# Optimization experiments

Hardware: AMD Instinct MI355X
Metric: run time of the kernel (lower is better)

## Reference

```python
import jax, jax.numpy as jnp
import numpy as np

B, P, Q, E, V = 8192, 24, 12, 256, 1000
LN_EPS = 1e-5


def setup_inputs() -> dict:
    key = jax.random.key(0)
    ks = jax.random.split(key, 9)
    s1 = 1.0  # Linear(1,E): fan_in=1 -> kaiming uniform bound = 1
    s2 = 1.0 / np.sqrt(E)
    return {
        "x_num": jax.random.normal(ks[0], (B, P), dtype=jnp.float32),
        "x_cat": jax.random.randint(ks[1], (B, Q), 0, V, dtype=jnp.int64),
        "W1": jax.random.uniform(ks[2], (P, E), jnp.float32, -s1, s1),   # per-attr Linear(1,E) weight
        "b1": jax.random.uniform(ks[3], (P, E), jnp.float32, -s1, s1),
        "W2": jax.random.uniform(ks[4], (P, E, E), jnp.float32, -s2, s2),  # per-attr Linear(E,E)
        "b2": jax.random.uniform(ks[5], (P, E), jnp.float32, -s2, s2),
        "emb": jax.random.normal(ks[6], (Q, V, E), dtype=jnp.float32),   # per-attr embedding tables
        "gamma": jnp.ones((E,), jnp.float32),
        "beta": jnp.zeros((E,), jnp.float32),
    }


def reference(x_num, x_cat, W1, b1, W2, b2, emb, gamma, beta):
    # Numeric attrs: scalar -> E (Linear), GELU, E -> E (Linear), all P attrs batched.
    h = x_num[:, :, None] * W1[None, :, :] + b1[None, :, :]           # [B,P,E]
    h = jax.nn.gelu(h, approximate=False)                              # torch nn.GELU default (erf)
    num_tok = jnp.einsum("bpe,pef->bpf", h, W2) + b2[None, :, :]     # [B,P,E]
    # Categorical attrs: per-attribute gather.
    cat_tok = emb[jnp.arange(Q)[None, :], x_cat]                       # [B,Q,E]
    tokens = jnp.concatenate([num_tok, cat_tok], axis=1)               # [B,P+Q,E]
    # LayerNorm over last dim.
    mu = jnp.mean(tokens, axis=-1, keepdims=True)
    var = jnp.mean(jnp.square(tokens - mu), axis=-1, keepdims=True)
    return (tokens - mu) * jax.lax.rsqrt(var + LN_EPS) * gamma + beta
```

## Files before the change

kernel.cpp:

```cpp
#include <hip/hip_runtime.h>
#include <hip/hip_bf16.h>
#include <math.h>

#define B_ 8192
#define P_ 24
#define Q_ 12
#define E_ 256
#define V_ 1000
#define TOK_ 36
#define NK_ 129
#define NI_ 128
#define KT_ 8
#define NKBLK_ 17
#define X0_ (-6.0f)
#define DX_ (12.0f / 128.0f)
#define INVDX_ (128.0f / 12.0f)
#define LN_EPS_ 1e-5f

typedef float vfloat4 __attribute__((ext_vector_type(4)));

__device__ __forceinline__ float gelu_exact(float u) {
    return 0.5f * u * (1.0f + erff(u * 0.70710678118654752f));
}

__global__ __launch_bounds__(256) void build_table(
        const float* __restrict__ W1, const float* __restrict__ b1,
        const float* __restrict__ W2, const float* __restrict__ b2,
        float* __restrict__ T) {
    int p = blockIdx.x / NKBLK_;
    int k0 = (blockIdx.x - p * NKBLK_) * KT_;
    int f = threadIdx.x;

    __shared__ float h[KT_][E_ + 4];

    float w = W1[p * E_ + f];
    float b1v = b1[p * E_ + f];
    #pragma unroll
    for (int k = 0; k < KT_; ++k) {
        float x = X0_ + (float)(k0 + k) * DX_;
        h[k][f] = gelu_exact(fmaf(x, w, b1v));
    }
    __syncthreads();

    float acc[KT_];
    float b2v = b2[p * E_ + f];
    #pragma unroll
    for (int k = 0; k < KT_; ++k) acc[k] = b2v;

    const float* W2p = W2 + (size_t)p * E_ * E_ + f;
    for (int e = 0; e < E_; e += 4) {
        float w0 = W2p[(size_t)(e + 0) * E_];
        float w1 = W2p[(size_t)(e + 1) * E_];
        float w2v = W2p[(size_t)(e + 2) * E_];
        float w3 = W2p[(size_t)(e + 3) * E_];
        #pragma unroll
        for (int k = 0; k < KT_; ++k) {
            float4 hv = *(const float4*)&h[k][e];
            acc[k] = fmaf(hv.x, w0, acc[k]);
            acc[k] = fmaf(hv.y, w1, acc[k]);
            acc[k] = fmaf(hv.z, w2v, acc[k]);
            acc[k] = fmaf(hv.w, w3, acc[k]);
        }
    }
    #pragma unroll
    for (int k = 0; k < KT_; ++k) {
        int kk = k0 + k;
        if (kk < NK_) T[((size_t)p * NK_ + kk) * E_ + f] = acc[k];
    }
}

__device__ __forceinline__ void ln_store(float4 v, float4 g, float4 bt, int e0, int row,
                                         float* __restrict__ out) {
    float s1 = v.x + v.y + v.z + v.w;
    #pragma unroll
    for (int m = 1; m < 64; m <<= 1) s1 += __shfl_xor(s1, m, 64);
    float mean = s1 * (1.0f / (float)E_);
    float dx = v.x - mean, dy = v.y - mean, dz = v.z - mean, dw = v.w - mean;
    float s2 = dx * dx + dy * dy + dz * dz + dw * dw;
    #pragma unroll
    for (int m = 1; m < 64; m <<= 1) s2 += __shfl_xor(s2, m, 64);
    float rstd = rsqrtf(s2 * (1.0f / (float)E_) + LN_EPS_);
    vfloat4 o;
    o.x = fmaf(dx * rstd, g.x, bt.x);
    o.y = fmaf(dy * rstd, g.y, bt.y);
    o.z = fmaf(dz * rstd, g.z, bt.z);
    o.w = fmaf(dw * rstd, g.w, bt.w);
    __builtin_nontemporal_store(o, (vfloat4*)&out[(size_t)row * E_ + e0]);
}

__global__ __launch_bounds__(256) void fuse_all(
        const float* __restrict__ T,
        const float* __restrict__ x_num, const int* __restrict__ x_cat,
        const float* __restrict__ emb,
        const float* __restrict__ gamma, const float* __restrict__ beta,
        float* __restrict__ out) {
    int wv = threadIdx.x >> 6;
    int lane = threadIdx.x & 63;
    int base = (blockIdx.x * 4 + wv) * 4;
    int b = base / TOK_;
    int t0 = base - b * TOK_;
    int e0 = lane * 4;

    float4 g = *(const float4*)&gamma[e0];
    float4 bt = *(const float4*)&beta[e0];

    float4 v[4];
    if (t0 < P_) {
        float4 x4 = *(const float4*)&x_num[b * P_ + t0];
        float xs[4] = {x4.x, x4.y, x4.z, x4.w};
        const float* bases[4];
        float tts[4];
        #pragma unroll
        for (int j = 0; j < 4; ++j) {
            float s = (xs[j] - X0_) * INVDX_;
            float fi = floorf(s);
            fi = fminf(fmaxf(fi, 0.0f), (float)(NI_ - 1));
            tts[j] = s - fi;
            bases[j] = T + ((size_t)(t0 + j) * NK_ + (int)fi) * E_ + e0;
        }
        float4 a[4], c[4];
        #pragma unroll
        for (int j = 0; j < 4; ++j) {
            a[j] = *(const float4*)bases[j];
            c[j] = *(const float4*)(bases[j] + E_);
        }
        #pragma unroll
        for (int j = 0; j < 4; ++j) {
            v[j].x = fmaf(tts[j], c[j].x - a[j].x, a[j].x);
            v[j].y = fmaf(tts[j], c[j].y - a[j].y, a[j].y);
            v[j].z = fmaf(tts[j], c[j].z - a[j].z, a[j].z);
            v[j].w = fmaf(tts[j], c[j].w - a[j].w, a[j].w);
        }
    } else {
        int q0 = t0 - P_;
        int4 id4 = *(const int4*)&x_cat[b * Q_ + q0];
        int ids[4] = {id4.x, id4.y, id4.z, id4.w};
        #pragma unroll
        for (int j = 0; j < 4; ++j)
            v[j] = *(const float4*)&emb[((size_t)(q0 + j) * V_ + ids[j]) * E_ + e0];
    }
    #pragma unroll
    for (int j = 0; j < 4; ++j) ln_store(v[j], g, bt, e0, base + j, out);
}

__global__ __launch_bounds__(256) void fuse_exact(
        const float* __restrict__ x_num, const int* __restrict__ x_cat,
        const float* __restrict__ W1, const float* __restrict__ b1,
        const float* __restrict__ W2, const float* __restrict__ b2,
        const float* __restrict__ emb,
        const float* __restrict__ gamma, const float* __restrict__ beta,
        float* __restrict__ out) {
    int wv = threadIdx.x >> 6;
    int lane = threadIdx.x & 63;
    int row = blockIdx.x * 4 + wv;
    if (row >= B_ * TOK_) return;
    int b = row / TOK_;
    int t = row - b * TOK_;
    int e0 = lane * 4;
    float4 g = *(const float4*)&gamma[e0];
    float4 bt = *(const float4*)&beta[e0];
    float4 v;
    if (t < P_) {
        float x = x_num[b * P_ + t];
        float4 acc = *(const float4*)&b2[t * E_ + e0];
        for (int e = 0; e < E_; ++e) {
            float he = gelu_exact(fmaf(x, W1[t * E_ + e], b1[t * E_ + e]));
            float4 w = *(const float4*)&W2[((size_t)t * E_ + e) * E_ + e0];
            acc.x = fmaf(he, w.x, acc.x);
            acc.y = fmaf(he, w.y, acc.y);
            acc.z = fmaf(he, w.z, acc.z);
            acc.w = fmaf(he, w.w, acc.w);
        }
        v = acc;
    } else {
        int q = t - P_;
        int idx = x_cat[b * Q_ + q];
        v = *(const float4*)&emb[((size_t)q * V_ + idx) * E_ + e0];
    }
    ln_store(v, g, bt, e0, row, out);
}

extern "C" void kernel_launch(void* const* d_in, const int* in_sizes, int n_in,
                              void* d_out, int out_size, void* d_ws, size_t ws_size,
                              hipStream_t stream) {
    const float* x_num = (const float*)d_in[0];
    const int*   x_cat = (const int*)d_in[1];
    const float* W1    = (const float*)d_in[2];
    const float* b1    = (const float*)d_in[3];
    const float* W2    = (const float*)d_in[4];
    const float* b2    = (const float*)d_in[5];
    const float* emb   = (const float*)d_in[6];
    const float* gamma = (const float*)d_in[7];
    const float* beta  = (const float*)d_in[8];
    float* out = (float*)d_out;

    size_t tbl_bytes = (size_t)P_ * NK_ * E_ * sizeof(float);

    if (ws_size >= tbl_bytes) {
        float* Tbl = (float*)d_ws;
        build_table<<<P_ * NKBLK_, 256, 0, stream>>>(W1, b1, W2, b2, Tbl);
        int nblocks = (B_ * TOK_) / 16;
        fuse_all<<<nblocks, 256, 0, stream>>>(Tbl, x_num, x_cat, emb, gamma, beta, out);
    } else {
        int nrow_blocks = (B_ * TOK_ + 3) / 4;
        fuse_exact<<<nrow_blocks, 256, 0, stream>>>(x_num, x_cat, W1, b1, W2, b2,
                                                    emb, gamma, beta, out);
    }
}
```

Measured before the change: 83.74 us.

## Precompute LayerNorm statistics per table interval and embedding row

Per-row LayerNorm statistics are now precomputed. Each embedding row gets its sum and sum of squares, and each interpolation interval gets the moments sa, sc, saa, scc and sac, so the main kernel computes mean and variance in closed form without wave-wide shuffle reductions. The main kernel becomes a grid-stride loop over 2048 blocks, and the embedding stats are computed inside the table-build launch. This adds one extra kernel launch and an E[x^2]-mean^2 variance formula that is less numerically robust, in exchange for removing the per-row shuffle reductions.

New measurement: 86.89 us. 3.8% more time.

```diff
diff --git a/kernel.cpp b/kernel.cpp
--- a/kernel.cpp
+++ b/kernel.cpp
@@ -12,10 +12,15 @@
 #define NI_ 128
 #define KT_ 8
 #define NKBLK_ 17
+#define NBUILD_ (P_ * NKBLK_)
+#define NEMBROW_ (Q_ * V_)
+#define NEMB_BLK_ ((NEMBROW_ + 3) / 4)
+#define NTILE_ ((B_ * TOK_) / 16)
 #define X0_ (-6.0f)
 #define DX_ (12.0f / 128.0f)
 #define INVDX_ (128.0f / 12.0f)
 #define LN_EPS_ 1e-5f
+#define INV_E_ (1.0f / 256.0f)
 
 typedef float vfloat4 __attribute__((ext_vector_type(4)));
 
@@ -23,124 +28,166 @@
     return 0.5f * u * (1.0f + erff(u * 0.70710678118654752f));
 }
 
-__global__ __launch_bounds__(256) void build_table(
+__device__ __forceinline__ float wave_sum(float x) {
+    #pragma unroll
+    for (int m = 1; m < 64; m <<= 1) x += __shfl_xor(x, m, 64);
+    return x;
+}
+
+__global__ __launch_bounds__(256) void build_and_embstats(
         const float* __restrict__ W1, const float* __restrict__ b1,
         const float* __restrict__ W2, const float* __restrict__ b2,
-        float* __restrict__ T) {
-    int p = blockIdx.x / NKBLK_;
-    int k0 = (blockIdx.x - p * NKBLK_) * KT_;
-    int f = threadIdx.x;
-
+        const float* __restrict__ emb,
+        float* __restrict__ T, float* __restrict__ ES) {
     __shared__ float h[KT_][E_ + 4];
 
-    float w = W1[p * E_ + f];
-    float b1v = b1[p * E_ + f];
-    #pragma unroll
-    for (int k = 0; k < KT_; ++k) {
-        float x = X0_ + (float)(k0 + k) * DX_;
-        h[k][f] = gelu_exact(fmaf(x, w, b1v));
-    }
-    __syncthreads();
-
-    float acc[KT_];
-    float b2v = b2[p * E_ + f];
-    #pragma unroll
-    for (int k = 0; k < KT_; ++k) acc[k] = b2v;
-
-    const float* W2p = W2 + (size_t)p * E_ * E_ + f;
-    for (int e = 0; e < E_; e += 4) {
-        float w0 = W2p[(size_t)(e + 0) * E_];
-        float w1 = W2p[(size_t)(e + 1) * E_];
-        float w2v = W2p[(size_t)(e + 2) * E_];
-        float w3 = W2p[(size_t)(e + 3) * E_];
+    if (blockIdx.x < NBUILD_) {
+        int p = blockIdx.x / NKBLK_;
+        int k0 = (blockIdx.x - p * NKBLK_) * KT_;
+        int f = threadIdx.x;
+
+        float w = W1[p * E_ + f];
+        float b1v = b1[p * E_ + f];
         #pragma unroll
         for (int k = 0; k < KT_; ++k) {
-            float4 hv = *(const float4*)&h[k][e];
-            acc[k] = fmaf(hv.x, w0, acc[k]);
-            acc[k] = fmaf(hv.y, w1, acc[k]);
-            acc[k] = fmaf(hv.z, w2v, acc[k]);
-            acc[k] = fmaf(hv.w, w3, acc[k]);
-        }
-    }
-    #pragma unroll
-    for (int k = 0; k < KT_; ++k) {
-        int kk = k0 + k;
-        if (kk < NK_) T[((size_t)p * NK_ + kk) * E_ + f] = acc[k];
-    }
-}
-
-__device__ __forceinline__ void ln_store(float4 v, float4 g, float4 bt, int e0, int row,
-                                         float* __restrict__ out) {
-    float s1 = v.x + v.y + v.z + v.w;
-    #pragma unroll
-    for (int m = 1; m < 64; m <<= 1) s1 += __shfl_xor(s1, m, 64);
-    float mean = s1 * (1.0f / (float)E_);
-    float dx = v.x - mean, dy = v.y - mean, dz = v.z - mean, dw = v.w - mean;
-    float s2 = dx * dx + dy * dy + dz * dz + dw * dw;
-    #pragma unroll
-    for (int m = 1; m < 64; m <<= 1) s2 += __shfl_xor(s2, m, 64);
-    float rstd = rsqrtf(s2 * (1.0f / (float)E_) + LN_EPS_);
-    vfloat4 o;
-    o.x = fmaf(dx * rstd, g.x, bt.x);
-    o.y = fmaf(dy * rstd, g.y, bt.y);
-    o.z = fmaf(dz * rstd, g.z, bt.z);
-    o.w = fmaf(dw * rstd, g.w, bt.w);
-    __builtin_nontemporal_store(o, (vfloat4*)&out[(size_t)row * E_ + e0]);
-}
-
-__global__ __launch_bounds__(256) void fuse_all(
-        const float* __restrict__ T,
+            float x = X0_ + (float)(k0 + k) * DX_;
+            h[k][f] = gelu_exact(fmaf(x, w, b1v));
+        }
+        __syncthreads();
+
+        float acc[KT_];
+        float b2v = b2[p * E_ + f];
+        #pragma unroll
+        for (int k = 0; k < KT_; ++k) acc[k] = b2v;
+
+        const float* W2p = W2 + (size_t)p * E_ * E_ + f;
+        for (int e = 0; e < E_; e += 4) {
+            float w0 = W2p[(size_t)(e + 0) * E_];
+            float w1 = W2p[(size_t)(e + 1) * E_];
+            float w2v = W2p[(size_t)(e + 2) * E_];
+            float w3 = W2p[(size_t)(e + 3) * E_];
+            #pragma unroll
+            for (int k = 0; k < KT_; ++k) {
+                float4 hv = *(const float4*)&h[k][e];
+                acc[k] = fmaf(hv.x, w0, acc[k]);
+                acc[k] = fmaf(hv.y, w1, acc[k]);
+                acc[k] = fmaf(hv.z, w2v, acc[k]);
+                acc[k] = fmaf(hv.w, w3, acc[k]);
+            }
+        }
+        #pragma unroll
+        for (int k = 0; k < KT_; ++k) {
+            int kk = k0 + k;
+            if (kk < NK_) T[((size_t)p * NK_ + kk) * E_ + f] = acc[k];
+        }
+    } else {
+        int wv = threadIdx.x >> 6;
+        int lane = threadIdx.x & 63;
+        int r = (blockIdx.x - NBUILD_) * 4 + wv;
+        if (r >= NEMBROW_) return;
+        float4 e4 = *(const float4*)&emb[(size_t)r * E_ + lane * 4];
+        float s1 = e4.x + e4.y + e4.z + e4.w;
+        float s2 = e4.x * e4.x + e4.y * e4.y + e4.z * e4.z + e4.w * e4.w;
+        s1 = wave_sum(s1);
+        s2 = wave_sum(s2);
+        if (lane == 0) { ES[r * 2] = s1; ES[r * 2 + 1] = s2; }
+    }
+}
+
+__global__ __launch_bounds__(256) void interval_stats(
+        const float* __restrict__ T, float* __restrict__ IS) {
+    int wv = threadIdx.x >> 6;
+    int lane = threadIdx.x & 63;
+    int m = blockIdx.x * 4 + wv;
+    if (m >= P_ * NI_) return;
+    int p = m >> 7;
+    int i = m & 127;
+    const float* rowa = T + ((size_t)p * NK_ + i) * E_ + lane * 4;
+    float4 a = *(const float4*)rowa;
+    float4 c = *(const float4*)(rowa + E_);
+    float sa = a.x + a.y + a.z + a.w;
+    float sc = c.x + c.y + c.z + c.w;
+    float saa = a.x * a.x + a.y * a.y + a.z * a.z + a.w * a.w;
+    float scc = c.x * c.x + c.y * c.y + c.z * c.z + c.w * c.w;
+    float sac = a.x * c.x + a.y * c.y + a.z * c.z + a.w * c.w;
+    sa = wave_sum(sa); sc = wave_sum(sc);
+    saa = wave_sum(saa); scc = wave_sum(scc); sac = wave_sum(sac);
+    if (lane == 0) {
+        float* o = IS + (size_t)m * 8;
+        o[0] = sa; o[1] = sc; o[2] = saa; o[3] = scc; o[4] = sac;
+        o[5] = 0.f; o[6] = 0.f; o[7] = 0.f;
+    }
+}
+
+__global__ __launch_bounds__(256) void fuse_stream(
+        const float* __restrict__ T, const float* __restrict__ IS,
+        const float* __restrict__ ES,
         const float* __restrict__ x_num, const int* __restrict__ x_cat,
         const float* __restrict__ emb,
         const float* __restrict__ gamma, const float* __restrict__ beta,
         float* __restrict__ out) {
     int wv = threadIdx.x >> 6;
     int lane = threadIdx.x & 63;
-    int base = (blockIdx.x * 4 + wv) * 4;
-    int b = base / TOK_;
-    int t0 = base - b * TOK_;
     int e0 = lane * 4;
-
     float4 g = *(const float4*)&gamma[e0];
     float4 bt = *(const float4*)&beta[e0];
 
-    float4 v[4];
-    if (t0 < P_) {
-        float4 x4 = *(const float4*)&x_num[b * P_ + t0];
-        float xs[4] = {x4.x, x4.y, x4.z, x4.w};
-        const float* bases[4];
-        float tts[4];
-        #pragma unroll
-        for (int j = 0; j < 4; ++j) {
-            float s = (xs[j] - X0_) * INVDX_;
-            float fi = floorf(s);
-            fi = fminf(fmaxf(fi, 0.0f), (float)(NI_ - 1));
-            tts[j] = s - fi;
-            bases[j] = T + ((size_t)(t0 + j) * NK_ + (int)fi) * E_ + e0;
-        }
-        float4 a[4], c[4];
-        #pragma unroll
-        for (int j = 0; j < 4; ++j) {
-            a[j] = *(const float4*)bases[j];
-            c[j] = *(const float4*)(bases[j] + E_);
-        }
-        #pragma unroll
-        for (int j = 0; j < 4; ++j) {
-            v[j].x = fmaf(tts[j], c[j].x - a[j].x, a[j].x);
-            v[j].y = fmaf(tts[j], c[j].y - a[j].y, a[j].y);
-            v[j].z = fmaf(tts[j], c[j].z - a[j].z, a[j].z);
-            v[j].w = fmaf(tts[j], c[j].w - a[j].w, a[j].w);
-        }
-    } else {
-        int q0 = t0 - P_;
-        int4 id4 = *(const int4*)&x_cat[b * Q_ + q0];
-        int ids[4] = {id4.x, id4.y, id4.z, id4.w};
-        #pragma unroll
-        for (int j = 0; j < 4; ++j)
-            v[j] = *(const float4*)&emb[((size_t)(q0 + j) * V_ + ids[j]) * E_ + e0];
-    }
-    #pragma unroll
-    for (int j = 0; j < 4; ++j) ln_store(v[j], g, bt, e0, base + j, out);
+    for (int tile = blockIdx.x; tile < NTILE_; tile += gridDim.x) {
+        int base = tile * 16 + wv * 4;
+        int b = base / TOK_;
+        int t0 = base - b * TOK_;
+        if (t0 < P_) {
+            float4 x4 = *(const float4*)&x_num[b * P_ + t0];
+            float xs[4] = {x4.x, x4.y, x4.z, x4.w};
+            #pragma unroll
+            for (int j = 0; j < 4; ++j) {
+                float s = (xs[j] - X0_) * INVDX_;
+                float fi = floorf(s);
+                fi = fminf(fmaxf(fi, 0.0f), (float)(NI_ - 1));
+                float t = s - fi;
+                int i = (int)fi;
+                int pp = t0 + j;
+                const float* rowa = T + ((size_t)pp * NK_ + i) * E_ + e0;
+                float4 a = *(const float4*)rowa;
+                float4 c = *(const float4*)(rowa + E_);
+                const float* ist = IS + ((size_t)pp * NI_ + i) * 8;
+                float4 q1 = *(const float4*)ist;
+                float sac = ist[4];
+                float u = 1.0f - t;
+                float mean = fmaf(t, q1.y - q1.x, q1.x) * INV_E_;
+                float m2 = (u * u * q1.z + 2.0f * t * u * sac + t * t * q1.w) * INV_E_;
+                float rstd = rsqrtf(fmaxf(m2 - mean * mean, 0.0f) + LN_EPS_);
+                vfloat4 o;
+                float vx = fmaf(t, c.x - a.x, a.x);
+                float vy = fmaf(t, c.y - a.y, a.y);
+                float vz = fmaf(t, c.z - a.z, a.z);
+                float vw = fmaf(t, c.w - a.w, a.w);
+                o.x = fmaf((vx - mean) * rstd, g.x, bt.x);
+                o.y = fmaf((vy - mean) * rstd, g.y, bt.y);
+                o.z = fmaf((vz - mean) * rstd, g.z, bt.z);
+                o.w = fmaf((vw - mean) * rstd, g.w, bt.w);
+                __builtin_nontemporal_store(o, (vfloat4*)&out[(size_t)(base + j) * E_ + e0]);
+            }
+        } else {
+            int q0 = t0 - P_;
+            int4 id4 = *(const int4*)&x_cat[b * Q_ + q0];
+            int ids[4] = {id4.x, id4.y, id4.z, id4.w};
+            #pragma unroll
+            for (int j = 0; j < 4; ++j) {
+                int r = (q0 + j) * V_ + ids[j];
+                float4 e4 = *(const float4*)&emb[(size_t)r * E_ + e0];
+                float s1 = ES[r * 2], s2 = ES[r * 2 + 1];
+                float mean = s1 * INV_E_;
+                float rstd = rsqrtf(fmaxf(s2 * INV_E_ - mean * mean, 0.0f) + LN_EPS_);
+                vfloat4 o;
+                o.x = fmaf((e4.x - mean) * rstd, g.x, bt.x);
+                o.y = fmaf((e4.y - mean) * rstd, g.y, bt.y);
+                o.z = fmaf((e4.z - mean) * rstd, g.z, bt.z);
+                o.w = fmaf((e4.w - mean) * rstd, g.w, bt.w);
+                __builtin_nontemporal_store(o, (vfloat4*)&out[(size_t)(base + j) * E_ + e0]);
+            }
+        }
+    }
 }
 
 __global__ __launch_bounds__(256) void fuse_exact(
@@ -177,7 +224,17 @@
         int idx = x_cat[b * Q_ + q];
         v = *(const float4*)&emb[((size_t)q * V_ + idx) * E_ + e0];
     }
-    ln_store(v, g, bt, e0, row, out);
+    float s1 = wave_sum(v.x + v.y + v.z + v.w);
+    float mean = s1 * INV_E_;
+    float dx = v.x - mean, dy = v.y - mean, dz = v.z - mean, dw = v.w - mean;
+    float s2 = wave_sum(dx * dx + dy * dy + dz * dz + dw * dw);
+    float rstd = rsqrtf(s2 * INV_E_ + LN_EPS_);
+    vfloat4 o;
+    o.x = fmaf(dx * rstd, g.x, bt.x);
+    o.y = fmaf(dy * rstd, g.y, bt.y);
+    o.z = fmaf(dz * rstd, g.z, bt.z);
+    o.w = fmaf(dw * rstd, g.w, bt.w);
+    __builtin_nontemporal_store(o, (vfloat4*)&out[(size_t)row * E_ + e0]);
 }
 
 extern "C" void kernel_launch(void* const* d_in, const int* in_sizes, int n_in,
@@ -194,13 +251,20 @@
     const float* beta  = (const float*)d_in[8];
     float* out = (float*)d_out;
 
-    size_t tbl_bytes = (size_t)P_ * NK_ * E_ * sizeof(float);
-
-    if (ws_size >= tbl_bytes) {
+    size_t tbl_floats = (size_t)P_ * NK_ * E_;
+    size_t is_floats  = (size_t)P_ * NI_ * 8;
+    size_t es_floats  = (size_t)NEMBROW_ * 2;
+    size_t need = (tbl_floats + is_floats + es_floats) * sizeof(float);
+
+    if (ws_size >= need) {
         float* Tbl = (float*)d_ws;
-        build_table<<<P_ * NKBLK_, 256, 0, stream>>>(W1, b1, W2, b2, Tbl);
-        int nblocks = (B_ * TOK_) / 16;
-        fuse_all<<<nblocks, 256, 0, stream>>>(Tbl, x_num, x_cat, emb, gamma, beta, out);
+        float* IS  = Tbl + tbl_floats;
+        float* ES  = IS + is_floats;
+        build_and_embstats<<<NBUILD_ + NEMB_BLK_, 256, 0, stream>>>(
+            W1, b1, W2, b2, emb, Tbl, ES);
+        interval_stats<<<(P_ * NI_) / 4, 256, 0, stream>>>(Tbl, IS);
+        fuse_stream<<<2048, 256, 0, stream>>>(Tbl, IS, ES, x_num, x_cat, emb,
+                                              gamma, beta, out);
     } else {
         int nrow_blocks = (B_ * TOK_ + 3) / 4;
         fuse_exact<<<nrow_blocks, 256, 0, stream>>>(x_num, x_cat, W1, b1, W2, b2,
```

## Overlap table build with categorical rows via cooperative persistent kernel

Applied to the files above, without the earlier changes.

Merges the table-build and fuse kernels into one cooperative persistent kernel. Some blocks build the interpolation table while the rest handle the categorical embedding rows, then a grid-wide sync precedes the numeric interpolation rows. This hides the table build behind the gather-bound categorical work and removes one launch. In exchange it adds a grid barrier, host-side attribute queries on every call, and a grid of 1024 blocks that must all be co-resident.

Result: slower. 224.2 us (+167.7%).

```diff
diff --git a/kernel.cpp b/kernel.cpp
--- a/kernel.cpp
+++ b/kernel.cpp
@@ -1,4 +1,5 @@
 #include <hip/hip_runtime.h>
+#include <hip/hip_cooperative_groups.h>
 #include <hip/hip_bf16.h>
 #include <math.h>
 
@@ -12,10 +13,15 @@
 #define NI_ 128
 #define KT_ 8
 #define NKBLK_ 17
+#define NBUILD_ (P_ * NKBLK_)
+#define NCAT_TILES_ ((B_ * Q_) / 16)
+#define NNUM_TILES_ ((B_ * P_) / 16)
+#define GRID_ 1024
 #define X0_ (-6.0f)
 #define DX_ (12.0f / 128.0f)
 #define INVDX_ (128.0f / 12.0f)
 #define LN_EPS_ 1e-5f
+#define INV_E_ (1.0f / 256.0f)
 
 typedef float vfloat4 __attribute__((ext_vector_type(4)));
 
@@ -23,15 +29,33 @@
     return 0.5f * u * (1.0f + erff(u * 0.70710678118654752f));
 }
 
-__global__ __launch_bounds__(256) void build_table(
-        const float* __restrict__ W1, const float* __restrict__ b1,
-        const float* __restrict__ W2, const float* __restrict__ b2,
-        float* __restrict__ T) {
-    int p = blockIdx.x / NKBLK_;
-    int k0 = (blockIdx.x - p * NKBLK_) * KT_;
+__device__ __forceinline__ float wave_sum(float x) {
+    #pragma unroll
+    for (int m = 1; m < 64; m <<= 1) x += __shfl_xor(x, m, 64);
+    return x;
+}
+
+__device__ __forceinline__ void ln_store(float4 v, float4 g, float4 bt, int e0, int row,
+                                         float* __restrict__ out) {
+    float mean = wave_sum(v.x + v.y + v.z + v.w) * INV_E_;
+    float dx = v.x - mean, dy = v.y - mean, dz = v.z - mean, dw = v.w - mean;
+    float s2 = wave_sum(dx * dx + dy * dy + dz * dz + dw * dw);
+    float rstd = rsqrtf(s2 * INV_E_ + LN_EPS_);
+    vfloat4 o;
+    o.x = fmaf(dx * rstd, g.x, bt.x);
+    o.y = fmaf(dy * rstd, g.y, bt.y);
+    o.z = fmaf(dz * rstd, g.z, bt.z);
+    o.w = fmaf(dw * rstd, g.w, bt.w);
+    __builtin_nontemporal_store(o, (vfloat4*)&out[(size_t)row * E_ + e0]);
+}
+
+__device__ __forceinline__ void do_build_chunk(
+        int bid, const float* __restrict__ W1, const float* __restrict__ b1,
+        const float* __restrict__ W2, const float* __restrict__ b2,
+        float* __restrict__ T, float (*h)[E_ + 4]) {
+    int p = bid / NKBLK_;
+    int k0 = (bid - p * NKBLK_) * KT_;
     int f = threadIdx.x;
-
-    __shared__ float h[KT_][E_ + 4];
 
     float w = W1[p * E_ + f];
     float b1v = b1[p * E_ + f];
@@ -69,78 +93,117 @@
     }
 }
 
-__device__ __forceinline__ void ln_store(float4 v, float4 g, float4 bt, int e0, int row,
-                                         float* __restrict__ out) {
-    float s1 = v.x + v.y + v.z + v.w;
-    #pragma unroll
-    for (int m = 1; m < 64; m <<= 1) s1 += __shfl_xor(s1, m, 64);
-    float mean = s1 * (1.0f / (float)E_);
-    float dx = v.x - mean, dy = v.y - mean, dz = v.z - mean, dw = v.w - mean;
-    float s2 = dx * dx + dy * dy + dz * dz + dw * dw;
-    #pragma unroll
-    for (int m = 1; m < 64; m <<= 1) s2 += __shfl_xor(s2, m, 64);
-    float rstd = rsqrtf(s2 * (1.0f / (float)E_) + LN_EPS_);
-    vfloat4 o;
-    o.x = fmaf(dx * rstd, g.x, bt.x);
-    o.y = fmaf(dy * rstd, g.y, bt.y);
-    o.z = fmaf(dz * rstd, g.z, bt.z);
-    o.w = fmaf(dw * rstd, g.w, bt.w);
-    __builtin_nontemporal_store(o, (vfloat4*)&out[(size_t)row * E_ + e0]);
-}
-
-__global__ __launch_bounds__(256) void fuse_all(
-        const float* __restrict__ T,
+__device__ __forceinline__ void do_cat_tile(
+        int tile, int wv, int lane, const int* __restrict__ x_cat,
+        const float* __restrict__ emb, float4 g, float4 bt,
+        float* __restrict__ out) {
+    int r0 = tile * 16 + wv * 4;
+    int b = r0 / Q_;
+    int q0 = r0 - b * Q_;
+    int e0 = lane * 4;
+    int4 id4 = *(const int4*)&x_cat[b * Q_ + q0];
+    int ids[4] = {id4.x, id4.y, id4.z, id4.w};
+    float4 v[4];
+    #pragma unroll
+    for (int j = 0; j < 4; ++j)
+        v[j] = *(const float4*)&emb[((size_t)(q0 + j) * V_ + ids[j]) * E_ + e0];
+    int orow = b * TOK_ + P_ + q0;
+    #pragma unroll
+    for (int j = 0; j < 4; ++j) ln_store(v[j], g, bt, e0, orow + j, out);
+}
+
+__device__ __forceinline__ void do_num_tile(
+        int tile, int wv, int lane, const float* __restrict__ T,
+        const float* __restrict__ x_num, float4 g, float4 bt,
+        float* __restrict__ out) {
+    int r0 = tile * 16 + wv * 4;
+    int b = r0 / P_;
+    int t0 = r0 - b * P_;
+    int e0 = lane * 4;
+    float4 x4 = *(const float4*)&x_num[b * P_ + t0];
+    float xs[4] = {x4.x, x4.y, x4.z, x4.w};
+    const float* bases[4];
+    float tts[4];
+    #pragma unroll
+    for (int j = 0; j < 4; ++j) {
+        float s = (xs[j] - X0_) * INVDX_;
+        float fi = floorf(s);
+        fi = fminf(fmaxf(fi, 0.0f), (float)(NI_ - 1));
+        tts[j] = s - fi;
+        bases[j] = T + ((size_t)(t0 + j) * NK_ + (int)fi) * E_ + e0;
+    }
+    float4 a[4], c[4];
+    #pragma unroll
+    for (int j = 0; j < 4; ++j) {
+        a[j] = *(const float4*)bases[j];
+        c[j] = *(const float4*)(bases[j] + E_);
+    }
+    int orow = b * TOK_ + t0;
+    #pragma unroll
+    for (int j = 0; j < 4; ++j) {
+        float4 v;
+        v.x = fmaf(tts[j], c[j].x - a[j].x, a[j].x);
+        v.y = fmaf(tts[j], c[j].y - a[j].y, a[j].y);
+        v.z = fmaf(tts[j], c[j].z - a[j].z, a[j].z);
+        v.w = fmaf(tts[j], c[j].w - a[j].w, a[j].w);
+        ln_store(v, g, bt, e0, orow + j, out);
+    }
+}
+
+__global__ __launch_bounds__(256, 4) void mega(
+        const float* __restrict__ W1, const float* __restrict__ b1,
+        const float* __restrict__ W2, const float* __restrict__ b2,
         const float* __restrict__ x_num, const int* __restrict__ x_cat,
         const float* __restrict__ emb,
         const float* __restrict__ gamma, const float* __restrict__ beta,
-        float* __restrict__ out) {
-    int wv = threadIdx.x >> 6;
-    int lane = threadIdx.x & 63;
-    int base = (blockIdx.x * 4 + wv) * 4;
-    int b = base / TOK_;
-    int t0 = base - b * TOK_;
-    int e0 = lane * 4;
-
+        float* __restrict__ T, float* __restrict__ out) {
+    __shared__ float h[KT_][E_ + 4];
+    int wv = threadIdx.x >> 6;
+    int lane = threadIdx.x & 63;
+    int e0 = lane * 4;
     float4 g = *(const float4*)&gamma[e0];
     float4 bt = *(const float4*)&beta[e0];
 
-    float4 v[4];
-    if (t0 < P_) {
-        float4 x4 = *(const float4*)&x_num[b * P_ + t0];
-        float xs[4] = {x4.x, x4.y, x4.z, x4.w};
-        const float* bases[4];
-        float tts[4];
-        #pragma unroll
-        for (int j = 0; j < 4; ++j) {
-            float s = (xs[j] - X0_) * INVDX_;
-            float fi = floorf(s);
-            fi = fminf(fmaxf(fi, 0.0f), (float)(NI_ - 1));
-            tts[j] = s - fi;
-            bases[j] = T + ((size_t)(t0 + j) * NK_ + (int)fi) * E_ + e0;
-        }
-        float4 a[4], c[4];
-        #pragma unroll
-        for (int j = 0; j < 4; ++j) {
-            a[j] = *(const float4*)bases[j];
-            c[j] = *(const float4*)(bases[j] + E_);
-        }
-        #pragma unroll
-        for (int j = 0; j < 4; ++j) {
-            v[j].x = fmaf(tts[j], c[j].x - a[j].x, a[j].x);
-            v[j].y = fmaf(tts[j], c[j].y - a[j].y, a[j].y);
-            v[j].z = fmaf(tts[j], c[j].z - a[j].z, a[j].z);
-            v[j].w = fmaf(tts[j], c[j].w - a[j].w, a[j].w);
-        }
-    } else {
-        int q0 = t0 - P_;
-        int4 id4 = *(const int4*)&x_cat[b * Q_ + q0];
-        int ids[4] = {id4.x, id4.y, id4.z, id4.w};
-        #pragma unroll
-        for (int j = 0; j < 4; ++j)
-            v[j] = *(const float4*)&emb[((size_t)(q0 + j) * V_ + ids[j]) * E_ + e0];
-    }
-    #pragma unroll
-    for (int j = 0; j < 4; ++j) ln_store(v[j], g, bt, e0, base + j, out);
+    if (blockIdx.x < NBUILD_) {
+        do_build_chunk(blockIdx.x, W1, b1, W2, b2, T, h);
+    } else {
+        for (int t = blockIdx.x - NBUILD_; t < NCAT_TILES_; t += gridDim.x - NBUILD_)
+            do_cat_tile(t, wv, lane, x_cat, emb, g, bt, out);
+    }
+    cooperative_groups::this_grid().sync();
+    for (int t = blockIdx.x; t < NNUM_TILES_; t += gridDim.x)
+        do_num_tile(t, wv, lane, T, x_num, g, bt, out);
+}
+
+__global__ __launch_bounds__(256) void build_and_cat_fb(
+        const float* __restrict__ W1, const float* __restrict__ b1,
+        const float* __restrict__ W2, const float* __restrict__ b2,
+        const int* __restrict__ x_cat, const float* __restrict__ emb,
+        const float* __restrict__ gamma, const float* __restrict__ beta,
+        float* __restrict__ T, float* __restrict__ out) {
+    __shared__ float h[KT_][E_ + 4];
+    int wv = threadIdx.x >> 6;
+    int lane = threadIdx.x & 63;
+    int e0 = lane * 4;
+    if (blockIdx.x < NBUILD_) {
+        do_build_chunk(blockIdx.x, W1, b1, W2, b2, T, h);
+    } else {
+        float4 g = *(const float4*)&gamma[e0];
+        float4 bt = *(const float4*)&beta[e0];
+        do_cat_tile(blockIdx.x - NBUILD_, wv, lane, x_cat, emb, g, bt, out);
+    }
+}
+
+__global__ __launch_bounds__(256) void fuse_num_fb(
+        const float* __restrict__ T, const float* __restrict__ x_num,
+        const float* __restrict__ gamma, const float* __restrict__ beta,
+        float* __restrict__ out) {
+    int wv = threadIdx.x >> 6;
+    int lane = threadIdx.x & 63;
+    int e0 = lane * 4;
+    float4 g = *(const float4*)&gamma[e0];
+    float4 bt = *(const float4*)&beta[e0];
+    do_num_tile(blockIdx.x, wv, lane, T, x_num, g, bt, out);
 }
 
 __global__ __launch_bounds__(256) void fuse_exact(
@@ -198,9 +261,23 @@
 
     if (ws_size >= tbl_bytes) {
         float* Tbl = (float*)d_ws;
-        build_table<<<P_ * NKBLK_, 256, 0, stream>>>(W1, b1, W2, b2, Tbl);
-        int nblocks = (B_ * TOK_) / 16;
-        fuse_all<<<nblocks, 256, 0, stream>>>(Tbl, x_num, x_cat, emb, gamma, beta, out);
+        int coop = 0, dev = 0;
+        hipGetDevice(&dev);
+        hipDeviceGetAttribute(&coop, hipDeviceAttributeCooperativeLaunch, dev);
+        bool done = false;
+        if (coop) {
+            void* args[] = {(void*)&W1, (void*)&b1, (void*)&W2, (void*)&b2,
+                            (void*)&x_num, (void*)&x_cat, (void*)&emb,
+                            (void*)&gamma, (void*)&beta, (void*)&Tbl, (void*)&out};
+            hipError_t e = hipLaunchCooperativeKernel((const void*)mega, dim3(GRID_),
+                                                      dim3(256), args, 0, stream);
+            done = (e == hipSuccess);
+        }
+        if (!done) {
+            build_and_cat_fb<<<NBUILD_ + NCAT_TILES_, 256, 0, stream>>>(
+                W1, b1, W2, b2, x_cat, emb, gamma, beta, Tbl, out);
+            fuse_num_fb<<<NNUM_TILES_, 256, 0, stream>>>(Tbl, x_num, gamma, beta, out);
+        }
     } else {
         int nrow_blocks = (B_ * TOK_ + 3) / 4;
         fuse_exact<<<nrow_blocks, 256, 0, stream>>>(x_num, x_cat, W1, b1, W2, b2,
```

## Overlap categorical gather with table build and use 16-lane row LayerNorm

Applied to the files above, without the earlier changes.

The table-build kernel now also handles the categorical embedding rows in extra blocks, so the gather and LayerNorm for those rows overlap with the lookup-table construction. A second kernel handles only the numeric rows. LayerNorm is restructured so 16 lanes cover one row (16 floats each) with a one-pass sum and sum-of-squares reduction over 4 shuffle steps instead of two 6-step passes. Stores are no longer nontemporal. The one-pass variance formula trades some numerical robustness for fewer shuffles.

New measurement: 133.2 us. +59.1%, slower.

```diff
diff --git a/kernel.cpp b/kernel.cpp
--- a/kernel.cpp
+++ b/kernel.cpp
@@ -12,10 +12,14 @@
 #define NI_ 128
 #define KT_ 8
 #define NKBLK_ 17
+#define NBUILD_ (P_ * NKBLK_)
+#define NCAT_TILES_ ((B_ * Q_) / 16)
+#define NNUM_TILES_ ((B_ * P_) / 16)
 #define X0_ (-6.0f)
 #define DX_ (12.0f / 128.0f)
 #define INVDX_ (128.0f / 12.0f)
 #define LN_EPS_ 1e-5f
+#define INV_E_ (1.0f / 256.0f)
 
 typedef float vfloat4 __attribute__((ext_vector_type(4)));
 
@@ -23,15 +27,13 @@
     return 0.5f * u * (1.0f + erff(u * 0.70710678118654752f));
 }
 
-__global__ __launch_bounds__(256) void build_table(
-        const float* __restrict__ W1, const float* __restrict__ b1,
+__device__ __forceinline__ void do_build_chunk(
+        int bid, const float* __restrict__ W1, const float* __restrict__ b1,
         const float* __restrict__ W2, const float* __restrict__ b2,
-        float* __restrict__ T) {
-    int p = blockIdx.x / NKBLK_;
-    int k0 = (blockIdx.x - p * NKBLK_) * KT_;
+        float* __restrict__ T, float (*h)[E_ + 4]) {
+    int p = bid / NKBLK_;
+    int k0 = (bid - p * NKBLK_) * KT_;
     int f = threadIdx.x;
-
-    __shared__ float h[KT_][E_ + 4];
 
     float w = W1[p * E_ + f];
     float b1v = b1[p * E_ + f];
@@ -69,78 +71,120 @@
     }
 }
 
-__device__ __forceinline__ void ln_store(float4 v, float4 g, float4 bt, int e0, int row,
-                                         float* __restrict__ out) {
-    float s1 = v.x + v.y + v.z + v.w;
-    #pragma unroll
-    for (int m = 1; m < 64; m <<= 1) s1 += __shfl_xor(s1, m, 64);
-    float mean = s1 * (1.0f / (float)E_);
-    float dx = v.x - mean, dy = v.y - mean, dz = v.z - mean, dw = v.w - mean;
-    float s2 = dx * dx + dy * dy + dz * dz + dw * dw;
-    #pragma unroll
-    for (int m = 1; m < 64; m <<= 1) s2 += __shfl_xor(s2, m, 64);
-    float rstd = rsqrtf(s2 * (1.0f / (float)E_) + LN_EPS_);
-    vfloat4 o;
-    o.x = fmaf(dx * rstd, g.x, bt.x);
-    o.y = fmaf(dy * rstd, g.y, bt.y);
-    o.z = fmaf(dz * rstd, g.z, bt.z);
-    o.w = fmaf(dw * rstd, g.w, bt.w);
-    __builtin_nontemporal_store(o, (vfloat4*)&out[(size_t)row * E_ + e0]);
-}
-
-__global__ __launch_bounds__(256) void fuse_all(
-        const float* __restrict__ T,
-        const float* __restrict__ x_num, const int* __restrict__ x_cat,
-        const float* __restrict__ emb,
+__device__ __forceinline__ void ln16_store(
+        const float4 v[4], const float4 gg[4], const float4 bb[4],
+        int c, int row, float* __restrict__ out) {
+    float s1 = 0.f, ss = 0.f;
+    #pragma unroll
+    for (int j = 0; j < 4; ++j) {
+        s1 += v[j].x + v[j].y + v[j].z + v[j].w;
+        ss += v[j].x * v[j].x + v[j].y * v[j].y + v[j].z * v[j].z + v[j].w * v[j].w;
+    }
+    #pragma unroll
+    for (int m = 1; m < 16; m <<= 1) {
+        s1 += __shfl_xor(s1, m, 64);
+        ss += __shfl_xor(ss, m, 64);
+    }
+    float mean = s1 * INV_E_;
+    float var = fmaxf(ss * INV_E_ - mean * mean, 0.0f);
+    float rstd = rsqrtf(var + LN_EPS_);
+    float* orow = out + (size_t)row * E_ + c * 16;
+    #pragma unroll
+    for (int j = 0; j < 4; ++j) {
+        float4 o;
+        o.x = fmaf((v[j].x - mean) * rstd, gg[j].x, bb[j].x);
+        o.y = fmaf((v[j].y - mean) * rstd, gg[j].y, bb[j].y);
+        o.z = fmaf((v[j].z - mean) * rstd, gg[j].z, bb[j].z);
+        o.w = fmaf((v[j].w - mean) * rstd, gg[j].w, bb[j].w);
+        *(float4*)(orow + j * 4) = o;
+    }
+}
+
+__device__ __forceinline__ void do_cat_tile(
+        int tile, int wv, int r, int c, const int* __restrict__ x_cat,
+        const float* __restrict__ emb, const float4 gg[4], const float4 bb[4],
+        float* __restrict__ out) {
+    int r0 = tile * 16 + wv * 4;
+    int b = r0 / Q_;
+    int q0 = r0 - b * Q_;
+    int4 id4 = *(const int4*)&x_cat[b * Q_ + q0];
+    int idx = (r == 0) ? id4.x : (r == 1) ? id4.y : (r == 2) ? id4.z : id4.w;
+    const float* erow = emb + ((size_t)(q0 + r) * V_ + idx) * E_ + c * 16;
+    float4 v[4];
+    #pragma unroll
+    for (int j = 0; j < 4; ++j) v[j] = *(const float4*)(erow + j * 4);
+    ln16_store(v, gg, bb, c, b * TOK_ + P_ + q0 + r, out);
+}
+
+__device__ __forceinline__ void do_num_tile(
+        int tile, int wv, int r, int c, const float* __restrict__ T,
+        const float* __restrict__ x_num, const float4 gg[4], const float4 bb[4],
+        float* __restrict__ out) {
+    int r0 = tile * 16 + wv * 4;
+    int b = r0 / P_;
+    int t0 = r0 - b * P_;
+    float4 x4 = *(const float4*)&x_num[b * P_ + t0];
+    float x = (r == 0) ? x4.x : (r == 1) ? x4.y : (r == 2) ? x4.z : x4.w;
+    float s = (x - X0_) * INVDX_;
+    float fi = floorf(s);
+    fi = fminf(fmaxf(fi, 0.0f), (float)(NI_ - 1));
+    float t = s - fi;
+    int p = t0 + r;
+    const float* rowa = T + ((size_t)p * NK_ + (int)fi) * E_ + c * 16;
+    float4 a[4], cc[4];
+    #pragma unroll
+    for (int j = 0; j < 4; ++j) {
+        a[j] = *(const float4*)(rowa + j * 4);
+        cc[j] = *(const float4*)(rowa + E_ + j * 4);
+    }
+    float4 v[4];
+    #pragma unroll
+    for (int j = 0; j < 4; ++j) {
+        v[j].x = fmaf(t, cc[j].x - a[j].x, a[j].x);
+        v[j].y = fmaf(t, cc[j].y - a[j].y, a[j].y);
+        v[j].z = fmaf(t, cc[j].z - a[j].z, a[j].z);
+        v[j].w = fmaf(t, cc[j].w - a[j].w, a[j].w);
+    }
+    ln16_store(v, gg, bb, c, b * TOK_ + t0 + r, out);
+}
+
+__global__ __launch_bounds__(256) void build_and_cat(
+        const float* __restrict__ W1, const float* __restrict__ b1,
+        const float* __restrict__ W2, const float* __restrict__ b2,
+        const int* __restrict__ x_cat, const float* __restrict__ emb,
+        const float* __restrict__ gamma, const float* __restrict__ beta,
+        float* __restrict__ T, float* __restrict__ out) {
+    __shared__ float h[KT_][E_ + 4];
+    if (blockIdx.x < NBUILD_) {
+        do_build_chunk(blockIdx.x, W1, b1, W2, b2, T, h);
+    } else {
+        int wv = threadIdx.x >> 6;
+        int lane = threadIdx.x & 63;
+        int r = lane >> 4, c = lane & 15;
+        float4 gg[4], bb[4];
+        #pragma unroll
+        for (int j = 0; j < 4; ++j) {
+            gg[j] = *(const float4*)&gamma[c * 16 + j * 4];
+            bb[j] = *(const float4*)&beta[c * 16 + j * 4];
+        }
+        do_cat_tile(blockIdx.x - NBUILD_, wv, r, c, x_cat, emb, gg, bb, out);
+    }
+}
+
+__global__ __launch_bounds__(256) void fuse_num(
+        const float* __restrict__ T, const float* __restrict__ x_num,
         const float* __restrict__ gamma, const float* __restrict__ beta,
         float* __restrict__ out) {
     int wv = threadIdx.x >> 6;
     int lane = threadIdx.x & 63;
-    int base = (blockIdx.x * 4 + wv) * 4;
-    int b = base / TOK_;
-    int t0 = base - b * TOK_;
-    int e0 = lane * 4;
-
-    float4 g = *(const float4*)&gamma[e0];
-    float4 bt = *(const float4*)&beta[e0];
-
-    float4 v[4];
-    if (t0 < P_) {
-        float4 x4 = *(const float4*)&x_num[b * P_ + t0];
-        float xs[4] = {x4.x, x4.y, x4.z, x4.w};
-        const float* bases[4];
-        float tts[4];
-        #pragma unroll
-        for (int j = 0; j < 4; ++j) {
-            float s = (xs[j] - X0_) * INVDX_;
-            float fi = floorf(s);
-            fi = fminf(fmaxf(fi, 0.0f), (float)(NI_ - 1));
-            tts[j] = s - fi;
-            bases[j] = T + ((size_t)(t0 + j) * NK_ + (int)fi) * E_ + e0;
-        }
-        float4 a[4], c[4];
-        #pragma unroll
-        for (int j = 0; j < 4; ++j) {
-            a[j] = *(const float4*)bases[j];
-            c[j] = *(const float4*)(bases[j] + E_);
-        }
-        #pragma unroll
-        for (int j = 0; j < 4; ++j) {
-            v[j].x = fmaf(tts[j], c[j].x - a[j].x, a[j].x);
-            v[j].y = fmaf(tts[j], c[j].y - a[j].y, a[j].y);
-            v[j].z = fmaf(tts[j], c[j].z - a[j].z, a[j].z);
-            v[j].w = fmaf(tts[j], c[j].w - a[j].w, a[j].w);
-        }
-    } else {
-        int q0 = t0 - P_;
-        int4 id4 = *(const int4*)&x_cat[b * Q_ + q0];
-        int ids[4] = {id4.x, id4.y, id4.z, id4.w};
-        #pragma unroll
-        for (int j = 0; j < 4; ++j)
-            v[j] = *(const float4*)&emb[((size_t)(q0 + j) * V_ + ids[j]) * E_ + e0];
-    }
-    #pragma unroll
-    for (int j = 0; j < 4; ++j) ln_store(v[j], g, bt, e0, base + j, out);
+    int r = lane >> 4, c = lane & 15;
+    float4 gg[4], bb[4];
+    #pragma unroll
+    for (int j = 0; j < 4; ++j) {
+        gg[j] = *(const float4*)&gamma[c * 16 + j * 4];
+        bb[j] = *(const float4*)&beta[c * 16 + j * 4];
+    }
+    do_num_tile(blockIdx.x, wv, r, c, T, x_num, gg, bb, out);
 }
 
 __global__ __launch_bounds__(256) void fuse_exact(
@@ -177,7 +221,21 @@
         int idx = x_cat[b * Q_ + q];
         v = *(const float4*)&emb[((size_t)q * V_ + idx) * E_ + e0];
     }
-    ln_store(v, g, bt, e0, row, out);
+    float s1 = v.x + v.y + v.z + v.w;
+    #pragma unroll
+    for (int m = 1; m < 64; m <<= 1) s1 += __shfl_xor(s1, m, 64);
+    float mean = s1 * INV_E_;
+    float dx = v.x - mean, dy = v.y - mean, dz = v.z - mean, dw = v.w - mean;
+    float s2 = dx * dx + dy * dy + dz * dz + dw * dw;
+    #pragma unroll
+    for (int m = 1; m < 64; m <<= 1) s2 += __shfl_xor(s2, m, 64);
+    float rstd = rsqrtf(s2 * INV_E_ + LN_EPS_);
+    float4 o;
+    o.x = fmaf(dx * rstd, g.x, bt.x);
+    o.y = fmaf(dy * rstd, g.y, bt.y);
+    o.z = fmaf(dz * rstd, g.z, bt.z);
+    o.w = fmaf(dw * rstd, g.w, bt.w);
+    *(float4*)&out[(size_t)row * E_ + e0] = o;
 }
 
 extern "C" void kernel_launch(void* const* d_in, const int* in_sizes, int n_in,
@@ -198,9 +256,9 @@
 
     if (ws_size >= tbl_bytes) {
         float* Tbl = (float*)d_ws;
-        build_table<<<P_ * NKBLK_, 256, 0, stream>>>(W1, b1, W2, b2, Tbl);
-        int nblocks = (B_ * TOK_) / 16;
-        fuse_all<<<nblocks, 256, 0, stream>>>(Tbl, x_num, x_cat, emb, gamma, beta, out);
+        build_and_cat<<<NBUILD_ + NCAT_TILES_, 256, 0, stream>>>(
+            W1, b1, W2, b2, x_cat, emb, gamma, beta, Tbl, out);
+        fuse_num<<<NNUM_TILES_, 256, 0, stream>>>(Tbl, x_num, gamma, beta, out);
     } else {
         int nrow_blocks = (B_ * TOK_ + 3) / 4;
         fuse_exact<<<nrow_blocks, 256, 0, stream>>>(x_num, x_cat, W1, b1, W2, b2,
```
